# Kernel tuning notes

Measured on AMD Instinct MI355X. Metric: run time of the kernel, lower is better.

The kernel has to match this reference:

```python
import jax, jax.numpy as jnp
import numpy as np

B, S, H, I = 2, 1024, 1024, 4096
G, E = 4, 4
NE = G * E
CAP = 1024


def setup_inputs() -> dict:
    key = jax.random.key(0)
    ks = jax.random.split(key, 6)
    return {
        "hidden_states": jax.random.normal(ks[0], (B, S, H), jnp.float32),
        "group_router_w": jax.random.normal(ks[1], (G, H), jnp.float32) * 0.02,
        "expert_router_w": jax.random.normal(ks[2], (G, E, H), jnp.float32) * 0.02,
        "gate_w": jax.random.normal(ks[3], (NE, I, H), jnp.float32) * 0.02,
        "up_w": jax.random.normal(ks[4], (NE, I, H), jnp.float32) * 0.02,
        "down_w": jax.random.normal(ks[5], (NE, H, I), jnp.float32) * 0.02,
    }


def _forward(x, gw, erw, Wg, Wu, Wd):
    b, s, h = x.shape
    T = b * s
    xf = x.reshape(T, h)
    # level 1: group routing (fp32 softmax, top-2 groups)
    group_logits = xf @ gw.T                                        # [T,G]
    group_probs = jax.nn.softmax(group_logits.astype(jnp.float32), axis=-1)
    top_gp, top_gi = jax.lax.top_k(group_probs, 2)                  # [T,2]
    # level 2: per-group expert routing (top-1 expert within group)
    expert_logits = jnp.einsum('th,geh->tge', xf, erw)              # [T,G,E]
    expert_probs = jax.nn.softmax(expert_logits.astype(jnp.float32), axis=-1)
    e_idx = jnp.argmax(expert_probs, axis=-1)                       # [T,G]
    e_prob = jnp.max(expert_probs, axis=-1)                         # [T,G]
    sel_e = jnp.take_along_axis(e_idx, top_gi, axis=1)              # [T,2]
    sel_p = jnp.take_along_axis(e_prob, top_gi, axis=1)             # [T,2]
    eid = (top_gi * E + sel_e).reshape(-1)                          # [2T] global expert id
    wgt = (top_gp * sel_p).reshape(-1)                              # [2T] combine weight
    x2 = jnp.repeat(xf, 2, axis=0)                                  # [2T,H], slot-major per token
    # capacity-based dispatch: position within expert via cumsum of one-hot
    onehot = jax.nn.one_hot(eid, NE, dtype=jnp.int32)               # [2T,NE]
    pos = (jnp.cumsum(onehot, axis=0) * onehot).sum(axis=1) - 1     # [2T]
    keep = pos < CAP
    pos_c = jnp.where(keep, pos, CAP)                               # overflow -> dummy slot
    buf = jnp.zeros((NE, CAP + 1, h), x.dtype).at[eid, pos_c].set(x2)
    # grouped-GEMM gated FFN (SwiGLU) over all experts at once
    gate = jax.nn.silu(jnp.einsum('ech,eih->eci', buf, Wg))
    up = jnp.einsum('ech,eih->eci', buf, Wu)
    yexp = jnp.einsum('eci,ehi->ech', gate * up, Wd)                # [NE,CAP+1,H]
    # combine: gather back and weight; dropped tokens get zero weight
    y = yexp[eid, pos_c] * jnp.where(keep, wgt, 0.0)[:, None].astype(x.dtype)
    out = (y[0::2] + y[1::2]).reshape(b, s, h)
    aux_loss = jnp.zeros((), jnp.float32)  # aux-loss accumulation truncated in source; initialized to 0
    return out, aux_loss


def reference(hidden_states, group_router_w, expert_router_w, gate_w, up_w, down_w):
    return _forward(hidden_states, group_router_w, expert_router_w, gate_w, up_w, down_w)
```

## Files before the change

### kernel.cpp

```cpp
#include <hip/hip_runtime.h>
#include <hip/hip_bf16.h>

typedef float f32x4 __attribute__((ext_vector_type(4)));
typedef __bf16 bf16x8 __attribute__((ext_vector_type(8)));

#define H 1024
#define II 4096
#define NE 16
#define CAP 1024
#define NTOK 2048
#define NSLOT 4096

__global__ __launch_bounds__(256) void k_route(
    const float* __restrict__ x, const float* __restrict__ gw,
    const float* __restrict__ erw, int* __restrict__ eid,
    float* __restrict__ wgt) {
  int t = blockIdx.x * 4 + (threadIdx.x >> 6);
  int lane = threadIdx.x & 63;
  const float* xr = x + (size_t)t * H;
  double acc[20];
#pragma unroll
  for (int j = 0; j < 20; j++) acc[j] = 0.0;
  for (int it = 0; it < 16; ++it) {
    int h = it * 64 + lane;
    float xv = xr[h];
#pragma unroll
    for (int g = 0; g < 4; ++g) acc[g] += (double)xv * (double)gw[g * H + h];
#pragma unroll
    for (int j = 0; j < 16; ++j)
      acc[4 + j] += (double)xv * (double)erw[j * H + h];
  }
#pragma unroll
  for (int j = 0; j < 20; ++j) {
    double v = acc[j];
#pragma unroll
    for (int o = 32; o > 0; o >>= 1) v += __shfl_down(v, o, 64);
    acc[j] = v;
  }
  if (lane == 0) {
    float gl[4];
#pragma unroll
    for (int g = 0; g < 4; g++) gl[g] = (float)acc[g];
    int g1 = 0;
#pragma unroll
    for (int g = 1; g < 4; g++)
      if (gl[g] > gl[g1]) g1 = g;
    int g2 = (g1 == 0) ? 1 : 0;
#pragma unroll
    for (int g = 0; g < 4; g++)
      if (g != g1 && gl[g] > gl[g2]) g2 = g;
    float gm = fmaxf(fmaxf(gl[0], gl[1]), fmaxf(gl[2], gl[3]));
    float s = 0.f;
#pragma unroll
    for (int g = 0; g < 4; g++) s += expf(gl[g] - gm);
    float p[2] = {expf(gl[g1] - gm) / s, expf(gl[g2] - gm) / s};
    int gs[2] = {g1, g2};
#pragma unroll
    for (int k = 0; k < 2; k++) {
      int g = gs[k];
      float el[4];
#pragma unroll
      for (int e2 = 0; e2 < 4; e2++) el[e2] = (float)acc[4 + g * 4 + e2];
      int eb = 0;
#pragma unroll
      for (int e2 = 1; e2 < 4; e2++)
        if (el[e2] > el[eb]) eb = e2;
      float es = 0.f;
#pragma unroll
      for (int e2 = 0; e2 < 4; e2++) es += expf(el[e2] - el[eb]);
      eid[2 * t + k] = g * 4 + eb;
      wgt[2 * t + k] = p[k] * (1.f / es);
    }
  }
}

__global__ __launch_bounds__(1024) void k_scan(const int* __restrict__ eid,
                                               int* __restrict__ perm,
                                               int* __restrict__ cnt,
                                               int* __restrict__ kept) {
  int wid = threadIdx.x >> 6;
  int lane = threadIdx.x & 63;
  int ne[64];
#pragma unroll
  for (int it = 0; it < 64; ++it) ne[it] = eid[it * 64 + lane];
  int base = 0;
#pragma unroll
  for (int it = 0; it < 64; ++it) {
    int slot = it * 64 + lane;
    int e = ne[it];
    unsigned long long m = __ballot(e == wid);
    if (e == wid) {
      int pos = base + __popcll(m & ((1ull << lane) - 1ull));
      if (pos < CAP) {
        perm[wid * CAP + pos] = slot;
        kept[slot] = 1;
      } else {
        kept[slot] = 0;
      }
    }
    base += __popcll(m);
  }
  if (lane == 0) cnt[wid] = (base < CAP) ? base : CAP;
}

__global__ __launch_bounds__(256) void k_cvtx(const float* __restrict__ x,
                                              __bf16* __restrict__ xb) {
  size_t i = ((size_t)blockIdx.x * 256 + threadIdx.x) * 8;
  f32x4 a = *(const f32x4*)(x + i);
  f32x4 b = *(const f32x4*)(x + i + 4);
  bf16x8 o;
#pragma unroll
  for (int j = 0; j < 4; j++) {
    o[j] = (__bf16)a[j];
    o[j + 4] = (__bf16)b[j];
  }
  *(bf16x8*)(xb + i) = o;
}

#define FENCE_BAR()                                    \
  asm volatile("s_waitcnt lgkmcnt(0)" ::: "memory");   \
  __builtin_amdgcn_sched_barrier(0);                   \
  __builtin_amdgcn_s_barrier();

#define MFMA_BF16(A, B, C) __builtin_amdgcn_mfma_f32_16x16x32_bf16(A, B, C, 0, 0, 0)

#define ASTR 36

__global__ __launch_bounds__(256, 2) void k_gateup(
    const __bf16* __restrict__ xb, const float* __restrict__ Wg,
    const float* __restrict__ Wu, const int* __restrict__ perm,
    const int* __restrict__ cnt, __bf16* __restrict__ act) {
  __shared__ __bf16 As[2][128 * ASTR];
  __shared__ __bf16 Gs[2][64 * ASTR];
  __shared__ __bf16 Us[2][64 * ASTR];
  __shared__ int slotArr[128];
  const int e = blockIdx.z, nt = blockIdx.x, rt = blockIdx.y;
  const int ce = cnt[e];
  if (ce <= 0 || rt * 128 >= ce) return;
  const int tid = threadIdx.x, lane = tid & 63, wid = tid >> 6;
  if (tid < 128) {
    int ridx = rt * 128 + tid;
    slotArr[tid] = perm[e * CAP + (ridx < ce ? ridx : 0)];
  }
  __syncthreads();
  const int arow = tid >> 1, ahalf = tid & 1;
  const __bf16* pA = xb + (size_t)(slotArr[arow] >> 1) * H + ahalf * 16;
  const int wA = arow * ASTR + ahalf * 16;
  const int grow = tid >> 2, gq = tid & 3;
  const size_t ew = (size_t)e * II * H + (size_t)(nt * 64) * H;
  const float* pG = Wg + ew + (size_t)grow * H + gq * 8;
  const float* pU = Wu + ew + (size_t)grow * H + gq * 8;
  const int wG = grow * ASTR + gq * 8;
  const int wm = wid >> 1, wn = wid & 1;
  const int l15 = lane & 15, lk = lane >> 4;

  f32x4 accG[4][2], accU[4][2];
#pragma unroll
  for (int m = 0; m < 4; m++)
#pragma unroll
    for (int n = 0; n < 2; n++)
#pragma unroll
      for (int i = 0; i < 4; i++) {
        accG[m][n][i] = 0.f;
        accU[m][n][i] = 0.f;
      }

  bf16x8 SA[4][2];
  f32x4 SG[4][2], SU[4][2];

#define GU_LOAD(s, T)                           \
  {                                             \
    const int ko = (T) * 32;                    \
    SA[s][0] = *(const bf16x8*)(pA + ko);       \
    SA[s][1] = *(const bf16x8*)(pA + ko + 8);   \
    SG[s][0] = *(const f32x4*)(pG + ko);        \
    SG[s][1] = *(const f32x4*)(pG + ko + 4);    \
    SU[s][0] = *(const f32x4*)(pU + ko);        \
    SU[s][1] = *(const f32x4*)(pU + ko + 4);    \
  }
#define GU_WRITE(B, s)                               \
  {                                                  \
    *(bf16x8*)&As[B][wA] = SA[s][0];                 \
    *(bf16x8*)&As[B][wA + 8] = SA[s][1];             \
    bf16x8 fg, fu;                                   \
    _Pragma("unroll") for (int i = 0; i < 4; i++) {  \
      fg[i] = (__bf16)SG[s][0][i];                   \
      fg[i + 4] = (__bf16)SG[s][1][i];               \
      fu[i] = (__bf16)SU[s][0][i];                   \
      fu[i + 4] = (__bf16)SU[s][1][i];               \
    }                                                \
    *(bf16x8*)&Gs[B][wG] = fg;                       \
    *(bf16x8*)&Us[B][wG] = fu;                       \
  }
#define GU_COMPUTE(B)                                                  \
  {                                                                    \
    bf16x8 aF[4], gF[2], uF[2];                                        \
    _Pragma("unroll") for (int m = 0; m < 4; m++)                      \
        aF[m] = *(const bf16x8*)&As[B][(wm * 64 + m * 16 + l15) * ASTR + lk * 8]; \
    _Pragma("unroll") for (int n = 0; n < 2; n++) {                    \
      gF[n] = *(const bf16x8*)&Gs[B][(wn * 32 + n * 16 + l15) * ASTR + lk * 8];   \
      uF[n] = *(const bf16x8*)&Us[B][(wn * 32 + n * 16 + l15) * ASTR + lk * 8];   \
    }                                                                  \
    _Pragma("unroll") for (int m = 0; m < 4; m++)                      \
        _Pragma("unroll") for (int n = 0; n < 2; n++) {                \
      accG[m][n] = MFMA_BF16(aF[m], gF[n], accG[m][n]);                \
      accU[m][n] = MFMA_BF16(aF[m], uF[n], accU[m][n]);                \
    }                                                                  \
  }

  GU_LOAD(0, 0);
  GU_LOAD(1, 1);
  GU_LOAD(2, 2);
  GU_LOAD(3, 3);
  GU_WRITE(0, 0);
  GU_LOAD(0, 4);
  FENCE_BAR();
  for (int tb = 0; tb < 4; ++tb) {
#pragma unroll
    for (int j = 0; j < 8; ++j) {
      const int t = tb * 8 + j;
      const int s = (j + 1) & 3;
      const int buf = j & 1;
      if (t + 1 < 32) GU_WRITE(buf ^ 1, s);
      if (t + 5 < 32) GU_LOAD(s, t + 5);
      GU_COMPUTE(buf);
      if (t + 1 < 32) FENCE_BAR();
    }
  }
  const int colB = nt * 64 + wn * 32;
#pragma unroll
  for (int m = 0; m < 4; m++)
#pragma unroll
    for (int n = 0; n < 2; n++)
#pragma unroll
      for (int i = 0; i < 4; i++) {
        int row = wm * 64 + m * 16 + lk * 4 + i;
        if (rt * 128 + row < ce) {
          int slot = slotArr[row];
          float g = accG[m][n][i];
          float u = accU[m][n][i];
          float a = (g / (1.f + __expf(-g))) * u;
          act[(size_t)slot * II + colB + n * 16 + l15] = (__bf16)a;
        }
      }
}

__global__ __launch_bounds__(256, 3) void k_down(
    const __bf16* __restrict__ act, const float* __restrict__ Wd,
    const int* __restrict__ perm, const int* __restrict__ cnt,
    const float* __restrict__ wgt, float* __restrict__ yb0,
    float* __restrict__ yb1) {
  __shared__ __bf16 As[2][128 * ASTR];
  __shared__ __bf16 Ws[2][64 * ASTR];
  __shared__ int slotArr[128];
  const int e = blockIdx.z, nt = blockIdx.x;
  const int rt = blockIdx.y & 7, sk = blockIdx.y >> 3;
  const int ce = cnt[e];
  if (ce <= 0 || rt * 128 >= ce) return;
  const int tid = threadIdx.x, lane = tid & 63, wid = tid >> 6;
  if (tid < 128) {
    int ridx = rt * 128 + tid;
    slotArr[tid] = perm[e * CAP + (ridx < ce ? ridx : 0)];
  }
  __syncthreads();
  const int KB = sk * 2048;
  const int arow = tid >> 1, ahalf = tid & 1;
  const __bf16* pA = act + (size_t)slotArr[arow] * II + KB + ahalf * 16;
  const int wA = arow * ASTR + ahalf * 16;
  const int grow = tid >> 2, gq = tid & 3;
  const float* pW =
      Wd + (size_t)e * H * II + (size_t)(nt * 64 + grow) * II + KB + gq * 8;
  const int wW = grow * ASTR + gq * 8;
  const int wm = wid >> 1, wn = wid & 1;
  const int l15 = lane & 15, lk = lane >> 4;

  f32x4 acc[4][2];
#pragma unroll
  for (int m = 0; m < 4; m++)
#pragma unroll
    for (int n = 0; n < 2; n++)
#pragma unroll
      for (int i = 0; i < 4; i++) acc[m][n][i] = 0.f;

  bf16x8 SA[4][2];
  f32x4 SW[4][2];

#define DN_LOAD(s, T)                           \
  {                                             \
    const int ko = (T) * 32;                    \
    SA[s][0] = *(const bf16x8*)(pA + ko);       \
    SA[s][1] = *(const bf16x8*)(pA + ko + 8);   \
    SW[s][0] = *(const f32x4*)(pW + ko);        \
    SW[s][1] = *(const f32x4*)(pW + ko + 4);    \
  }
#define DN_WRITE(B, s)                               \
  {                                                  \
    *(bf16x8*)&As[B][wA] = SA[s][0];                 \
    *(bf16x8*)&As[B][wA + 8] = SA[s][1];             \
    bf16x8 fw;                                       \
    _Pragma("unroll") for (int i = 0; i < 4; i++) {  \
      fw[i] = (__bf16)SW[s][0][i];                   \
      fw[i + 4] = (__bf16)SW[s][1][i];               \
    }                                                \
    *(bf16x8*)&Ws[B][wW] = fw;                       \
  }
#define DN_COMPUTE(B)                                                  \
  {                                                                    \
    bf16x8 aF[4], wF[2];                                               \
    _Pragma("unroll") for (int m = 0; m < 4; m++)                      \
        aF[m] = *(const bf16x8*)&As[B][(wm * 64 + m * 16 + l15) * ASTR + lk * 8]; \
    _Pragma("unroll") for (int n = 0; n < 2; n++)                      \
        wF[n] = *(const bf16x8*)&Ws[B][(wn * 32 + n * 16 + l15) * ASTR + lk * 8]; \
    _Pragma("unroll") for (int m = 0; m < 4; m++)                      \
        _Pragma("unroll") for (int n = 0; n < 2; n++)                  \
            acc[m][n] = MFMA_BF16(aF[m], wF[n], acc[m][n]);            \
  }

  DN_LOAD(0, 0);
  DN_LOAD(1, 1);
  DN_LOAD(2, 2);
  DN_LOAD(3, 3);
  DN_WRITE(0, 0);
  DN_LOAD(0, 4);
  FENCE_BAR();
  for (int tb = 0; tb < 8; ++tb) {
#pragma unroll
    for (int j = 0; j < 8; ++j) {
      const int t = tb * 8 + j;
      const int s = (j + 1) & 3;
      const int buf = j & 1;
      if (t + 1 < 64) DN_WRITE(buf ^ 1, s);
      if (t + 5 < 64) DN_LOAD(s, t + 5);
      DN_COMPUTE(buf);
      if (t + 1 < 64) FENCE_BAR();
    }
  }
  float* yp = sk ? yb1 : yb0;
  const int colB = nt * 64 + wn * 32;
#pragma unroll
  for (int m = 0; m < 4; m++)
#pragma unroll
    for (int n = 0; n < 2; n++)
#pragma unroll
      for (int i = 0; i < 4; i++) {
        int row = wm * 64 + m * 16 + lk * 4 + i;
        if (rt * 128 + row < ce) {
          int slot = slotArr[row];
          yp[(size_t)slot * H + colB + n * 16 + l15] =
              wgt[slot] * acc[m][n][i];
        }
      }
}

__global__ __launch_bounds__(256) void k_combine(const float* __restrict__ y0p,
                                                 const float* __restrict__ y1p,
                                                 const int* __restrict__ kept,
                                                 float* __restrict__ out) {
  int t = blockIdx.x, tid = threadIdx.x;
  size_t o0 = (size_t)(2 * t) * H, o1 = (size_t)(2 * t + 1) * H;
  f32x4 a, b;
#pragma unroll
  for (int i = 0; i < 4; i++) {
    a[i] = 0.f;
    b[i] = 0.f;
  }
  if (kept[2 * t])
    a = ((const f32x4*)(y0p + o0))[tid] + ((const f32x4*)(y1p + o0))[tid];
  if (kept[2 * t + 1])
    b = ((const f32x4*)(y0p + o1))[tid] + ((const f32x4*)(y1p + o1))[tid];
  ((f32x4*)out)[(size_t)t * 256 + tid] = a + b;
  if (t == 0 && tid == 0) out[(size_t)NTOK * H] = 0.f;
}

extern "C" void kernel_launch(void* const* d_in, const int* in_sizes, int n_in,
                              void* d_out, int out_size, void* d_ws,
                              size_t ws_size, hipStream_t stream) {
  const float* x = (const float*)d_in[0];
  const float* gw = (const float*)d_in[1];
  const float* erw = (const float*)d_in[2];
  const float* Wg = (const float*)d_in[3];
  const float* Wu = (const float*)d_in[4];
  const float* Wd = (const float*)d_in[5];
  float* out = (float*)d_out;
  char* ws = (char*)d_ws;
  int* eid = (int*)(ws);
  float* wgt = (float*)(ws + (16 << 10));
  int* kept = (int*)(ws + (32 << 10));
  int* cnt = (int*)(ws + (48 << 10));
  int* perm = (int*)(ws + (64 << 10));
  size_t off = 128 << 10;
  __bf16* act = (__bf16*)(ws + off);
  off += (size_t)NSLOT * II * 2;
  float* yb0 = (float*)(ws + off);
  off += (size_t)NSLOT * H * 4;
  float* yb1 = (float*)(ws + off);
  off += (size_t)NSLOT * H * 4;
  __bf16* xb = (__bf16*)(ws + off);

  k_route<<<NTOK / 4, 256, 0, stream>>>(x, gw, erw, eid, wgt);
  k_scan<<<1, 1024, 0, stream>>>(eid, perm, cnt, kept);
  k_cvtx<<<NTOK * H / 8 / 256, 256, 0, stream>>>(x, xb);
  k_gateup<<<dim3(64, 8, 16), 256, 0, stream>>>(xb, Wg, Wu, perm, cnt, act);
  k_down<<<dim3(16, 16, 16), 256, 0, stream>>>(act, Wd, perm, cnt, wgt, yb0, yb1);
  k_combine<<<NTOK, 256, 0, stream>>>(yb0, yb1, kept, out);
}
```

Baseline: 402.8 us.

## Stage GEMM tiles via direct global-to-LDS loads with XOR swizzle

Both grouped GEMM kernels now copy tiles straight from global memory into LDS using global_load_lds, replacing the register-staged prefetch ring. Weights are kept as fp32 in LDS with an XOR-swizzled layout and converted to bf16 only when fragments are read for the MFMAs. The pipeline is simplified to double buffering paced by vmcnt waits, and occupancy hints are raised from 2 to 3 and from 3 to 4 blocks. This removes VGPR staging and the store-to-LDS path, at the cost of doubling LDS weight footprint and repeating the fp32-to-bf16 conversion in every wave that reads a fragment.

```diff
diff --git a/kernel.cpp b/kernel.cpp
--- a/kernel.cpp
+++ b/kernel.cpp
@@ -10,6 +10,12 @@
 #define CAP 1024
 #define NTOK 2048
 #define NSLOT 4096
+
+__device__ __forceinline__ void gload16(const void* g, void* l) {
+  __builtin_amdgcn_global_load_lds(
+      (const __attribute__((address_space(1))) unsigned*)g,
+      (__attribute__((address_space(3))) unsigned*)l, 16, 0, 0);
+}
 
 __global__ __launch_bounds__(256) void k_route(
     const float* __restrict__ x, const float* __restrict__ gw,
@@ -117,41 +123,44 @@
   *(bf16x8*)(xb + i) = o;
 }
 
-#define FENCE_BAR()                                    \
-  asm volatile("s_waitcnt lgkmcnt(0)" ::: "memory");   \
-  __builtin_amdgcn_sched_barrier(0);                   \
-  __builtin_amdgcn_s_barrier();
+#define VMCNT(N) asm volatile("s_waitcnt vmcnt(" #N ")" ::: "memory")
+#define LGK0 asm volatile("s_waitcnt lgkmcnt(0)" ::: "memory")
+#define SBAR()                           \
+  __builtin_amdgcn_sched_barrier(0);     \
+  __builtin_amdgcn_s_barrier();          \
+  __builtin_amdgcn_sched_barrier(0);
 
 #define MFMA_BF16(A, B, C) __builtin_amdgcn_mfma_f32_16x16x32_bf16(A, B, C, 0, 0, 0)
 
-#define ASTR 36
-
-__global__ __launch_bounds__(256, 2) void k_gateup(
+__global__ __launch_bounds__(256, 3) void k_gateup(
     const __bf16* __restrict__ xb, const float* __restrict__ Wg,
     const float* __restrict__ Wu, const int* __restrict__ perm,
     const int* __restrict__ cnt, __bf16* __restrict__ act) {
-  __shared__ __bf16 As[2][128 * ASTR];
-  __shared__ __bf16 Gs[2][64 * ASTR];
-  __shared__ __bf16 Us[2][64 * ASTR];
+  __shared__ __bf16 As[2][128 * 32];
+  __shared__ float Gs[2][64 * 32];
+  __shared__ float Us[2][64 * 32];
   __shared__ int slotArr[128];
   const int e = blockIdx.z, nt = blockIdx.x, rt = blockIdx.y;
   const int ce = cnt[e];
   if (ce <= 0 || rt * 128 >= ce) return;
-  const int tid = threadIdx.x, lane = tid & 63, wid = tid >> 6;
+  const int tid = threadIdx.x, lane = tid & 63, w = tid >> 6;
   if (tid < 128) {
     int ridx = rt * 128 + tid;
     slotArr[tid] = perm[e * CAP + (ridx < ce ? ridx : 0)];
   }
   __syncthreads();
-  const int arow = tid >> 1, ahalf = tid & 1;
-  const __bf16* pA = xb + (size_t)(slotArr[arow] >> 1) * H + ahalf * 16;
-  const int wA = arow * ASTR + ahalf * 16;
-  const int grow = tid >> 2, gq = tid & 3;
+  const int rA0 = 32 * w + (lane >> 2), rA1 = rA0 + 16;
+  const __bf16* gA0 =
+      xb + (size_t)(slotArr[rA0] >> 1) * H + (((lane & 3) ^ ((rA0 >> 1) & 3)) * 8);
+  const __bf16* gA1 =
+      xb + (size_t)(slotArr[rA1] >> 1) * H + (((lane & 3) ^ ((rA1 >> 1) & 3)) * 8);
+  const int rW0 = 16 * w + (lane >> 3), rW1 = rW0 + 8;
   const size_t ew = (size_t)e * II * H + (size_t)(nt * 64) * H;
-  const float* pG = Wg + ew + (size_t)grow * H + gq * 8;
-  const float* pU = Wu + ew + (size_t)grow * H + gq * 8;
-  const int wG = grow * ASTR + gq * 8;
-  const int wm = wid >> 1, wn = wid & 1;
+  const float* gG0 = Wg + ew + (size_t)rW0 * H + (((lane & 7) ^ (rW0 & 7)) * 4);
+  const float* gG1 = Wg + ew + (size_t)rW1 * H + (((lane & 7) ^ (rW1 & 7)) * 4);
+  const float* gU0 = Wu + ew + (size_t)rW0 * H + (((lane & 7) ^ (rW0 & 7)) * 4);
+  const float* gU1 = Wu + ew + (size_t)rW1 * H + (((lane & 7) ^ (rW1 & 7)) * 4);
+  const int wm = w >> 1, wn = w & 1;
   const int l15 = lane & 15, lk = lane >> 4;
 
   f32x4 accG[4][2], accU[4][2];
@@ -165,68 +174,58 @@
         accU[m][n][i] = 0.f;
       }
 
-  bf16x8 SA[4][2];
-  f32x4 SG[4][2], SU[4][2];
-
-#define GU_LOAD(s, T)                           \
-  {                                             \
-    const int ko = (T) * 32;                    \
-    SA[s][0] = *(const bf16x8*)(pA + ko);       \
-    SA[s][1] = *(const bf16x8*)(pA + ko + 8);   \
-    SG[s][0] = *(const f32x4*)(pG + ko);        \
-    SG[s][1] = *(const f32x4*)(pG + ko + 4);    \
-    SU[s][0] = *(const f32x4*)(pU + ko);        \
-    SU[s][1] = *(const f32x4*)(pU + ko + 4);    \
-  }
-#define GU_WRITE(B, s)                               \
-  {                                                  \
-    *(bf16x8*)&As[B][wA] = SA[s][0];                 \
-    *(bf16x8*)&As[B][wA + 8] = SA[s][1];             \
-    bf16x8 fg, fu;                                   \
-    _Pragma("unroll") for (int i = 0; i < 4; i++) {  \
-      fg[i] = (__bf16)SG[s][0][i];                   \
-      fg[i + 4] = (__bf16)SG[s][1][i];               \
-      fu[i] = (__bf16)SU[s][0][i];                   \
-      fu[i + 4] = (__bf16)SU[s][1][i];               \
-    }                                                \
-    *(bf16x8*)&Gs[B][wG] = fg;                       \
-    *(bf16x8*)&Us[B][wG] = fu;                       \
-  }
-#define GU_COMPUTE(B)                                                  \
-  {                                                                    \
-    bf16x8 aF[4], gF[2], uF[2];                                        \
-    _Pragma("unroll") for (int m = 0; m < 4; m++)                      \
-        aF[m] = *(const bf16x8*)&As[B][(wm * 64 + m * 16 + l15) * ASTR + lk * 8]; \
-    _Pragma("unroll") for (int n = 0; n < 2; n++) {                    \
-      gF[n] = *(const bf16x8*)&Gs[B][(wn * 32 + n * 16 + l15) * ASTR + lk * 8];   \
-      uF[n] = *(const bf16x8*)&Us[B][(wn * 32 + n * 16 + l15) * ASTR + lk * 8];   \
-    }                                                                  \
-    _Pragma("unroll") for (int m = 0; m < 4; m++)                      \
-        _Pragma("unroll") for (int n = 0; n < 2; n++) {                \
-      accG[m][n] = MFMA_BF16(aF[m], gF[n], accG[m][n]);                \
-      accU[m][n] = MFMA_BF16(aF[m], uF[n], accU[m][n]);                \
-    }                                                                  \
-  }
-
-  GU_LOAD(0, 0);
-  GU_LOAD(1, 1);
-  GU_LOAD(2, 2);
-  GU_LOAD(3, 3);
-  GU_WRITE(0, 0);
-  GU_LOAD(0, 4);
-  FENCE_BAR();
-  for (int tb = 0; tb < 4; ++tb) {
-#pragma unroll
-    for (int j = 0; j < 8; ++j) {
-      const int t = tb * 8 + j;
-      const int s = (j + 1) & 3;
-      const int buf = j & 1;
-      if (t + 1 < 32) GU_WRITE(buf ^ 1, s);
-      if (t + 5 < 32) GU_LOAD(s, t + 5);
-      GU_COMPUTE(buf);
-      if (t + 1 < 32) FENCE_BAR();
-    }
-  }
+#define GU_STAGE(B, T)                                   \
+  {                                                      \
+    const int ko = (T) * 32;                             \
+    gload16(gA0 + ko, &As[B][(32 * w) * 32]);            \
+    gload16(gA1 + ko, &As[B][(32 * w + 16) * 32]);       \
+    gload16(gG0 + ko, &Gs[B][(16 * w) * 32]);            \
+    gload16(gG1 + ko, &Gs[B][(16 * w + 8) * 32]);        \
+    gload16(gU0 + ko, &Us[B][(16 * w) * 32]);            \
+    gload16(gU1 + ko, &Us[B][(16 * w + 8) * 32]);        \
+  }
+#define GU_COMPUTE(B)                                                       \
+  {                                                                         \
+    bf16x8 aF[4];                                                           \
+    _Pragma("unroll") for (int m = 0; m < 4; m++) {                         \
+      int r = wm * 64 + m * 16 + l15;                                       \
+      aF[m] = *(const bf16x8*)&As[B][r * 32 + ((lk ^ ((r >> 1) & 3)) * 8)]; \
+    }                                                                       \
+    _Pragma("unroll") for (int n = 0; n < 2; n++) {                         \
+      int r = wn * 32 + n * 16 + l15;                                       \
+      int cA = (2 * lk) ^ (r & 7), cB = cA ^ 1;                             \
+      f32x4 glo = *(const f32x4*)&Gs[B][r * 32 + cA * 4];                   \
+      f32x4 ghi = *(const f32x4*)&Gs[B][r * 32 + cB * 4];                   \
+      f32x4 ulo = *(const f32x4*)&Us[B][r * 32 + cA * 4];                   \
+      f32x4 uhi = *(const f32x4*)&Us[B][r * 32 + cB * 4];                   \
+      bf16x8 gF, uF;                                                        \
+      _Pragma("unroll") for (int i = 0; i < 4; i++) {                       \
+        gF[i] = (__bf16)glo[i];                                             \
+        gF[i + 4] = (__bf16)ghi[i];                                         \
+        uF[i] = (__bf16)ulo[i];                                             \
+        uF[i + 4] = (__bf16)uhi[i];                                         \
+      }                                                                     \
+      _Pragma("unroll") for (int m = 0; m < 4; m++) {                       \
+        accG[m][n] = MFMA_BF16(aF[m], gF, accG[m][n]);                      \
+        accU[m][n] = MFMA_BF16(aF[m], uF, accU[m][n]);                      \
+      }                                                                     \
+    }                                                                       \
+  }
+
+  GU_STAGE(0, 0);
+  GU_STAGE(1, 1);
+  for (int t = 0; t < 31; ++t) {
+    VMCNT(6);
+    SBAR();
+    GU_COMPUTE(t & 1);
+    LGK0;
+    SBAR();
+    if (t + 2 < 32) GU_STAGE(t & 1, t + 2);
+  }
+  VMCNT(0);
+  SBAR();
+  GU_COMPUTE(1);
+
   const int colB = nt * 64 + wn * 32;
 #pragma unroll
   for (int m = 0; m < 4; m++)
@@ -245,33 +244,36 @@
       }
 }
 
-__global__ __launch_bounds__(256, 3) void k_down(
+__global__ __launch_bounds__(256, 4) void k_down(
     const __bf16* __restrict__ act, const float* __restrict__ Wd,
     const int* __restrict__ perm, const int* __restrict__ cnt,
     const float* __restrict__ wgt, float* __restrict__ yb0,
     float* __restrict__ yb1) {
-  __shared__ __bf16 As[2][128 * ASTR];
-  __shared__ __bf16 Ws[2][64 * ASTR];
+  __shared__ __bf16 As[2][128 * 32];
+  __shared__ float Ws[2][64 * 32];
   __shared__ int slotArr[128];
   const int e = blockIdx.z, nt = blockIdx.x;
   const int rt = blockIdx.y & 7, sk = blockIdx.y >> 3;
   const int ce = cnt[e];
   if (ce <= 0 || rt * 128 >= ce) return;
-  const int tid = threadIdx.x, lane = tid & 63, wid = tid >> 6;
+  const int tid = threadIdx.x, lane = tid & 63, w = tid >> 6;
   if (tid < 128) {
     int ridx = rt * 128 + tid;
     slotArr[tid] = perm[e * CAP + (ridx < ce ? ridx : 0)];
   }
   __syncthreads();
   const int KB = sk * 2048;
-  const int arow = tid >> 1, ahalf = tid & 1;
-  const __bf16* pA = act + (size_t)slotArr[arow] * II + KB + ahalf * 16;
-  const int wA = arow * ASTR + ahalf * 16;
-  const int grow = tid >> 2, gq = tid & 3;
-  const float* pW =
-      Wd + (size_t)e * H * II + (size_t)(nt * 64 + grow) * II + KB + gq * 8;
-  const int wW = grow * ASTR + gq * 8;
-  const int wm = wid >> 1, wn = wid & 1;
+  const int rA0 = 32 * w + (lane >> 2), rA1 = rA0 + 16;
+  const __bf16* gA0 =
+      act + (size_t)slotArr[rA0] * II + KB + (((lane & 3) ^ ((rA0 >> 1) & 3)) * 8);
+  const __bf16* gA1 =
+      act + (size_t)slotArr[rA1] * II + KB + (((lane & 3) ^ ((rA1 >> 1) & 3)) * 8);
+  const int rW0 = 16 * w + (lane >> 3), rW1 = rW0 + 8;
+  const float* gW0 = Wd + (size_t)e * H * II + (size_t)(nt * 64 + rW0) * II + KB +
+                     (((lane & 7) ^ (rW0 & 7)) * 4);
+  const float* gW1 = Wd + (size_t)e * H * II + (size_t)(nt * 64 + rW1) * II + KB +
+                     (((lane & 7) ^ (rW1 & 7)) * 4);
+  const int wm = w >> 1, wn = w & 1;
   const int l15 = lane & 15, lk = lane >> 4;
 
   f32x4 acc[4][2];
@@ -282,59 +284,50 @@
 #pragma unroll
       for (int i = 0; i < 4; i++) acc[m][n][i] = 0.f;
 
-  bf16x8 SA[4][2];
-  f32x4 SW[4][2];
-
-#define DN_LOAD(s, T)                           \
-  {                                             \
-    const int ko = (T) * 32;                    \
-    SA[s][0] = *(const bf16x8*)(pA + ko);       \
-    SA[s][1] = *(const bf16x8*)(pA + ko + 8);   \
-    SW[s][0] = *(const f32x4*)(pW + ko);        \
-    SW[s][1] = *(const f32x4*)(pW + ko + 4);    \
-  }
-#define DN_WRITE(B, s)                               \
-  {                                                  \
-    *(bf16x8*)&As[B][wA] = SA[s][0];                 \
-    *(bf16x8*)&As[B][wA + 8] = SA[s][1];             \
-    bf16x8 fw;                                       \
-    _Pragma("unroll") for (int i = 0; i < 4; i++) {  \
-      fw[i] = (__bf16)SW[s][0][i];                   \
-      fw[i + 4] = (__bf16)SW[s][1][i];               \
-    }                                                \
-    *(bf16x8*)&Ws[B][wW] = fw;                       \
-  }
-#define DN_COMPUTE(B)                                                  \
-  {                                                                    \
-    bf16x8 aF[4], wF[2];                                               \
-    _Pragma("unroll") for (int m = 0; m < 4; m++)                      \
-        aF[m] = *(const bf16x8*)&As[B][(wm * 64 + m * 16 + l15) * ASTR + lk * 8]; \
-    _Pragma("unroll") for (int n = 0; n < 2; n++)                      \
-        wF[n] = *(const bf16x8*)&Ws[B][(wn * 32 + n * 16 + l15) * ASTR + lk * 8]; \
-    _Pragma("unroll") for (int m = 0; m < 4; m++)                      \
-        _Pragma("unroll") for (int n = 0; n < 2; n++)                  \
-            acc[m][n] = MFMA_BF16(aF[m], wF[n], acc[m][n]);            \
-  }
-
-  DN_LOAD(0, 0);
-  DN_LOAD(1, 1);
-  DN_LOAD(2, 2);
-  DN_LOAD(3, 3);
-  DN_WRITE(0, 0);
-  DN_LOAD(0, 4);
-  FENCE_BAR();
-  for (int tb = 0; tb < 8; ++tb) {
-#pragma unroll
-    for (int j = 0; j < 8; ++j) {
-      const int t = tb * 8 + j;
-      const int s = (j + 1) & 3;
-      const int buf = j & 1;
-      if (t + 1 < 64) DN_WRITE(buf ^ 1, s);
-      if (t + 5 < 64) DN_LOAD(s, t + 5);
-      DN_COMPUTE(buf);
-      if (t + 1 < 64) FENCE_BAR();
-    }
-  }
+#define DN_STAGE(B, T)                                   \
+  {                                                      \
+    const int ko = (T) * 32;                             \
+    gload16(gA0 + ko, &As[B][(32 * w) * 32]);            \
+    gload16(gA1 + ko, &As[B][(32 * w + 16) * 32]);       \
+    gload16(gW0 + ko, &Ws[B][(16 * w) * 32]);            \
+    gload16(gW1 + ko, &Ws[B][(16 * w + 8) * 32]);        \
+  }
+#define DN_COMPUTE(B)                                                       \
+  {                                                                         \
+    bf16x8 aF[4];                                                           \
+    _Pragma("unroll") for (int m = 0; m < 4; m++) {                         \
+      int r = wm * 64 + m * 16 + l15;                                       \
+      aF[m] = *(const bf16x8*)&As[B][r * 32 + ((lk ^ ((r >> 1) & 3)) * 8)]; \
+    }                                                                       \
+    _Pragma("unroll") for (int n = 0; n < 2; n++) {                         \
+      int r = wn * 32 + n * 16 + l15;                                       \
+      int cA = (2 * lk) ^ (r & 7), cB = cA ^ 1;                             \
+      f32x4 wlo = *(const f32x4*)&Ws[B][r * 32 + cA * 4];                   \
+      f32x4 whi = *(const f32x4*)&Ws[B][r * 32 + cB * 4];                   \
+      bf16x8 wF;                                                            \
+      _Pragma("unroll") for (int i = 0; i < 4; i++) {                       \
+        wF[i] = (__bf16)wlo[i];                                             \
+        wF[i + 4] = (__bf16)whi[i];                                         \
+      }                                                                     \
+      _Pragma("unroll") for (int m = 0; m < 4; m++)                         \
+          acc[m][n] = MFMA_BF16(aF[m], wF, acc[m][n]);                      \
+    }                                                                       \
+  }
+
+  DN_STAGE(0, 0);
+  DN_STAGE(1, 1);
+  for (int t = 0; t < 63; ++t) {
+    VMCNT(4);
+    SBAR();
+    DN_COMPUTE(t & 1);
+    LGK0;
+    SBAR();
+    if (t + 2 < 64) DN_STAGE(t & 1, t + 2);
+  }
+  VMCNT(0);
+  SBAR();
+  DN_COMPUTE(1);
+
   float* yp = sk ? yb1 : yb0;
   const int colB = nt * 64 + wn * 32;
 #pragma unroll
```

Measured after the change: 405.5 us. Within noise of the previous version (+0.7%).
